# Performance work log

Measured on AMD Instinct MI355X. Metric: run time of the kernel, lower is better.

## Reference

```python
import jax, jax.numpy as jnp
import numpy as np

EPS = 1e-5


def gcn_conv(x, edge_index, W, b):
    # PyG GCNConv: h = x @ W; add self-loops; symmetric deg^-1/2 normalization; scatter-add to dst; + bias
    n = x.shape[0]
    h = x @ W  # [N, out]
    loops = jnp.arange(n, dtype=edge_index.dtype)
    src = jnp.concatenate([edge_index[0], loops])
    dst = jnp.concatenate([edge_index[1], loops])
    deg = jax.ops.segment_sum(jnp.ones(src.shape[0], dtype=h.dtype), dst, num_segments=n)
    dinv = jnp.where(deg > 0, jax.lax.rsqrt(jnp.maximum(deg, 1e-12)), 0.0)
    norm = dinv[src] * dinv[dst]  # [E+N]
    out = jax.ops.segment_sum(h[src] * norm[:, None], dst, num_segments=n)
    return out + b


def setup_inputs() -> dict:
    key = jax.random.key(0)
    ks = jax.random.split(key, 10)
    N, E = 50000, 800000
    IN, HID, OUT = 128, 128, 64
    x = jax.random.normal(ks[0], (N, IN), dtype=jnp.float32)
    edge_index1 = jax.random.randint(ks[1], (2, E), 0, N, dtype=jnp.int64)
    edge_index2 = jax.random.randint(ks[2], (2, E), 0, N, dtype=jnp.int64)
    s1 = 1.0 / np.sqrt(IN)
    s2 = 1.0 / np.sqrt(HID)
    W1 = jax.random.uniform(ks[3], (IN, HID), jnp.float32, -s1, s1)
    b1 = jax.random.uniform(ks[4], (HID,), jnp.float32, -s1, s1)
    gamma = jnp.ones((HID,), jnp.float32)
    beta = jnp.zeros((HID,), jnp.float32)
    W2 = jax.random.uniform(ks[5], (HID, OUT), jnp.float32, -s2, s2)
    b2 = jax.random.uniform(ks[6], (OUT,), jnp.float32, -s2, s2)
    return {"x": x, "edge_index1": edge_index1, "edge_index2": edge_index2,
            "W1": W1, "b1": b1, "gamma": gamma, "beta": beta, "W2": W2, "b2": b2}


def reference(x, edge_index1, edge_index2, W1, b1, gamma, beta, W2, b2):
    # layer 1: GCNConv -> (save hidden) -> BatchNorm1d (batch stats) -> ReLU -> dropout (identity, deterministic)
    h = gcn_conv(x, edge_index1, W1, b1)
    hidden = h
    mean = jnp.mean(h, axis=0)
    var = jnp.mean((h - mean) ** 2, axis=0)  # biased var, as torch BN uses for normalization
    h = (h - mean) * jax.lax.rsqrt(var + EPS) * gamma + beta
    h = jax.nn.relu(h)
    # layer 2: GCNConv (no norm/act on last layer)
    out = gcn_conv(h, edge_index2, W2, b2)
    return (out, hidden)
```

## Files before the change

kernel.cpp:

```cpp
#include <hip/hip_runtime.h>

#define GN 50000
#define GE 800000
#define HID 128
#define OUTC 64
#define NBK 196
#define NW  196
#define EPW 4096
#define PCAP 5888
#define A1B 2048

#define OFF_H1    0
#define OFF_H2    3200000
#define OFF_DINV1 4800000
#define OFF_DINV2 4850000
#define OFF_ROW1  4900000
#define OFF_ROW2  4950004
#define OFF_HIST  5000008
#define OFF_TOT   5076840
#define OFF_BBASE 5077232
#define OFF_BN    5077632
#define OFF_PART  5078144
#define OFF_PARTA 5602432
#define OFF_SRC1  5606528
#define OFF_SRC2  6406528

typedef __attribute__((ext_vector_type(8))) short bf16x8;
typedef __attribute__((ext_vector_type(4))) float f32x4;

__device__ inline unsigned bf16rne(float f) {
  unsigned u = __float_as_uint(f);
  return (u + 0x7FFFu + ((u >> 16) & 1u)) >> 16;
}
__device__ inline unsigned pack2(float a, float b) {
  return bf16rne(a) | (bf16rne(b) << 16);
}
__device__ inline float bflo(unsigned w) { return __uint_as_float(w << 16); }
__device__ inline float bfhi(unsigned w) { return __uint_as_float(w & 0xFFFF0000u); }
__device__ inline float bfs(unsigned short w) { return __uint_as_float(((unsigned)w) << 16); }

__global__ __launch_bounds__(256) void p1hist_kernel(const int* __restrict__ e1,
    const int* __restrict__ e2, int* __restrict__ hist) {
  __shared__ int h[NBK];
  int g = blockIdx.y, w = blockIdx.x;
  const int* dst = (g ? e2 : e1) + GE;
  for (int i = threadIdx.x; i < NBK; i += 256) h[i] = 0;
  __syncthreads();
  int i0 = w * EPW, iend = i0 + EPW; if (iend > GE) iend = GE;
  for (int i = i0 + threadIdx.x; i < iend; i += 256)
    atomicAdd(&h[dst[i] >> 8], 1);
  __syncthreads();
  int* out = hist + ((size_t)g * NW + w) * NBK;
  for (int i = threadIdx.x; i < NBK; i += 256) out[i] = h[i];
}

__global__ __launch_bounds__(256) void histscanA_kernel(int* __restrict__ hist,
    int* __restrict__ tot) {
  __shared__ int lds[256];
  int b = blockIdx.x, g = blockIdx.y, t = threadIdx.x;
  int* col = hist + (size_t)g * NW * NBK + b;
  int v = (t < NW) ? col[(size_t)t * NBK] : 0;
  lds[t] = v;
  __syncthreads();
  for (int off = 1; off < 256; off <<= 1) {
    int u = (t >= off) ? lds[t - off] : 0;
    __syncthreads();
    lds[t] += u;
    __syncthreads();
  }
  if (t < NW) col[(size_t)t * NBK] = lds[t] - v;
  if (t == NW - 1) tot[g * NBK + b] = lds[t];
}

__global__ __launch_bounds__(256) void histscanB_kernel(const int* __restrict__ tot,
    int* __restrict__ bbase) {
  __shared__ int lds[256];
  int t = threadIdx.x;
  for (int g = 0; g < 2; ++g) {
    int v = (t < NBK) ? tot[g * NBK + t] : 0;
    int orig = v;
    lds[t] = v;
    __syncthreads();
    for (int off = 1; off < 256; off <<= 1) {
      int u = (t >= off) ? lds[t - off] : 0;
      __syncthreads();
      lds[t] += u;
      __syncthreads();
    }
    if (t < NBK) bbase[g * (NBK + 1) + t] = lds[t] - orig;
    if (t == NBK - 1) bbase[g * (NBK + 1) + NBK] = lds[t];
    __syncthreads();
  }
}

__global__ __launch_bounds__(256) void p1scat_kernel(const int* __restrict__ e1,
    const int* __restrict__ e2, const int* __restrict__ hist,
    const int* __restrict__ bbase, int* __restrict__ pb1, int* __restrict__ pb2) {
  __shared__ int off[NBK];
  int g = blockIdx.y, w = blockIdx.x;
  const int* e = g ? e2 : e1;
  int* pb = g ? pb2 : pb1;
  const int* hrow = hist + ((size_t)g * NW + w) * NBK;
  const int* bb = bbase + g * (NBK + 1);
  for (int i = threadIdx.x; i < NBK; i += 256) off[i] = bb[i] + hrow[i];
  __syncthreads();
  int i0 = w * EPW, iend = i0 + EPW; if (iend > GE) iend = GE;
  for (int i = i0 + threadIdx.x; i < iend; i += 256) {
    int d = e[GE + i], s = e[i];
    int p = atomicAdd(&off[d >> 8], 1);
    pb[p] = s | ((d & 255) << 16);
  }
}

__global__ __launch_bounds__(256) void p2sort_kernel(const int* __restrict__ pb1,
    const int* __restrict__ pb2, const int* __restrict__ bbase,
    int* __restrict__ row1, int* __restrict__ row2,
    float* __restrict__ dinv1, float* __restrict__ dinv2,
    int* __restrict__ src1, int* __restrict__ src2) {
  __shared__ int stage[PCAP];
  __shared__ int lcnt[256], lc2[256], arr[256];
  __shared__ int lrow[257];
  int g = blockIdx.y, b = blockIdx.x, t = threadIdx.x;
  const int* pb = g ? pb2 : pb1;
  const int* bb = bbase + g * (NBK + 1);
  int* row = g ? row2 : row1;
  float* dinv = g ? dinv2 : dinv1;
  int* src = g ? src2 : src1;
  int lo = b << 8, hi = lo + 256; if (hi > GN) hi = GN;
  int nn = hi - lo;
  int base = bb[b], end = bb[b + 1], L = end - base;
  lcnt[t] = 0; lc2[t] = 0;
  __syncthreads();
  for (int i = base + t; i < end; i += 256)
    atomicAdd(&lcnt[((unsigned)pb[i]) >> 16], 1);
  __syncthreads();
  int v = lcnt[t];
  arr[t] = v;
  __syncthreads();
  for (int off = 1; off < 256; off <<= 1) {
    int u = (t >= off) ? arr[t - off] : 0;
    __syncthreads();
    arr[t] += u;
    __syncthreads();
  }
  lrow[t] = arr[t] - v;
  if (t == 255) lrow[256] = arr[255];
  __syncthreads();
  if (t < nn) {
    row[lo + t] = base + lrow[t];
    dinv[lo + t] = rsqrtf(1.0f + (float)lcnt[t]);
  }
  if (b == NBK - 1 && t == 0) row[GN] = end;
  if (L <= PCAP) {
    for (int i = base + t; i < end; i += 256) {
      unsigned p = (unsigned)pb[i];
      int ld = p >> 16;
      int rk = atomicAdd(&lc2[ld], 1);
      stage[lrow[ld] + rk] = (int)(p & 0xFFFFu);
    }
    __syncthreads();
    for (int i = t; i < L; i += 256) src[base + i] = stage[i];
  } else {
    for (int i = base + t; i < end; i += 256) {
      unsigned p = (unsigned)pb[i];
      int ld = p >> 16;
      int rk = atomicAdd(&lc2[ld], 1);
      src[base + lrow[ld] + rk] = (int)(p & 0xFFFFu);
    }
  }
}

__global__ __launch_bounds__(256) void gemm1_kernel(const float* __restrict__ A,
    const float* __restrict__ W1, const float* __restrict__ dinv1,
    unsigned short* __restrict__ h1u) {
  __shared__ unsigned a_lds[64 * 68];
  __shared__ unsigned w_lds[128 * 68];
  int t = threadIdx.x;
  int row0 = blockIdx.x * 64;
  for (int i = t; i < 128 * 64; i += 256) {
    int k2 = i >> 7, n = i & 127;
    w_lds[n * 68 + k2] = pack2(W1[(2 * k2) * 128 + n], W1[(2 * k2 + 1) * 128 + n]);
  }
  for (int i = t; i < 64 * 32; i += 256) {
    int m = i >> 5, k4 = i & 31;
    int gr = row0 + m;
    float4 v = (gr < GN) ? ((const float4*)A)[(size_t)gr * 32 + k4]
                         : make_float4(0.f, 0.f, 0.f, 0.f);
    unsigned* dst = &a_lds[m * 68 + k4 * 2];
    dst[0] = pack2(v.x, v.y);
    dst[1] = pack2(v.z, v.w);
  }
  __syncthreads();
  int lane = t & 63, w = t >> 6;
  int n16 = lane & 15, quad = lane >> 4;
  int mbase = (w & 1) * 32;
  int nbase = (w >> 1) * 64;
  f32x4 acc[2][4] = {};
  const unsigned short* als = (const unsigned short*)a_lds;
  const unsigned short* wls = (const unsigned short*)w_lds;
  #pragma unroll
  for (int ks = 0; ks < 4; ++ks) {
    int k0 = ks * 32 + quad * 8;
    bf16x8 a0 = *(const bf16x8*)(als + (mbase + n16) * 136 + k0);
    bf16x8 a1 = *(const bf16x8*)(als + (mbase + 16 + n16) * 136 + k0);
    #pragma unroll
    for (int nt = 0; nt < 4; ++nt) {
      bf16x8 bf = *(const bf16x8*)(wls + (nbase + nt * 16 + n16) * 136 + k0);
      acc[0][nt] = __builtin_amdgcn_mfma_f32_16x16x32_bf16(a0, bf, acc[0][nt], 0, 0, 0);
      acc[1][nt] = __builtin_amdgcn_mfma_f32_16x16x32_bf16(a1, bf, acc[1][nt], 0, 0, 0);
    }
  }
  #pragma unroll
  for (int mt = 0; mt < 2; ++mt) {
    #pragma unroll
    for (int r = 0; r < 4; ++r) {
      int row_g = row0 + mbase + mt * 16 + quad * 4 + r;
      if (row_g < GN) {
        float dv = dinv1[row_g];
        #pragma unroll
        for (int nt = 0; nt < 4; ++nt) {
          int col = nbase + nt * 16 + n16;
          h1u[(size_t)row_g * 128 + col] = (unsigned short)bf16rne(dv * acc[mt][nt][r]);
        }
      }
    }
  }
}

__global__ __launch_bounds__(256) void gemm2_kernel(const float* __restrict__ A,
    const float* __restrict__ W2, const float* __restrict__ scale,
    const float* __restrict__ shift, const float* __restrict__ dinv2,
    unsigned short* __restrict__ h2u) {
  __shared__ unsigned a_lds[64 * 68];
  __shared__ unsigned w_lds[64 * 68];
  __shared__ float sc[128], sh[128];
  int t = threadIdx.x;
  if (t < 128) { sc[t] = scale[t]; sh[t] = shift[t]; }
  int row0 = blockIdx.x * 64;
  for (int i = t; i < 64 * 64; i += 256) {
    int k2 = i >> 6, n = i & 63;
    w_lds[n * 68 + k2] = pack2(W2[(2 * k2) * 64 + n], W2[(2 * k2 + 1) * 64 + n]);
  }
  __syncthreads();
  for (int i = t; i < 64 * 32; i += 256) {
    int m = i >> 5, k4 = i & 31;
    int gr = row0 + m;
    float4 v = (gr < GN) ? ((const float4*)A)[(size_t)gr * 32 + k4]
                         : make_float4(0.f, 0.f, 0.f, 0.f);
    int c = k4 * 4;
    v.x = fmaxf(fmaf(v.x, sc[c],     sh[c]),     0.f);
    v.y = fmaxf(fmaf(v.y, sc[c + 1], sh[c + 1]), 0.f);
    v.z = fmaxf(fmaf(v.z, sc[c + 2], sh[c + 2]), 0.f);
    v.w = fmaxf(fmaf(v.w, sc[c + 3], sh[c + 3]), 0.f);
    unsigned* dst = &a_lds[m * 68 + k4 * 2];
    dst[0] = pack2(v.x, v.y);
    dst[1] = pack2(v.z, v.w);
  }
  __syncthreads();
  int lane = t & 63, w = t >> 6;
  int n16 = lane & 15, quad = lane >> 4;
  f32x4 acc[4] = {};
  const unsigned short* als = (const unsigned short*)a_lds;
  const unsigned short* wls = (const unsigned short*)w_lds;
  #pragma unroll
  for (int ks = 0; ks < 4; ++ks) {
    int k0 = ks * 32 + quad * 8;
    bf16x8 af = *(const bf16x8*)(als + (w * 16 + n16) * 136 + k0);
    #pragma unroll
    for (int nt = 0; nt < 4; ++nt) {
      bf16x8 bf = *(const bf16x8*)(wls + (nt * 16 + n16) * 136 + k0);
      acc[nt] = __builtin_amdgcn_mfma_f32_16x16x32_bf16(af, bf, acc[nt], 0, 0, 0);
    }
  }
  #pragma unroll
  for (int r = 0; r < 4; ++r) {
    int row_g = row0 + w * 16 + quad * 4 + r;
    if (row_g < GN) {
      float dv = dinv2[row_g];
      #pragma unroll
      for (int nt = 0; nt < 4; ++nt) {
        int col = nt * 16 + n16;
        h2u[(size_t)row_g * 64 + col] = (unsigned short)bf16rne(dv * acc[nt][r]);
      }
    }
  }
}

__global__ __launch_bounds__(256) void agg1_kernel(const unsigned* __restrict__ h1b,
    const int* __restrict__ row, const int* __restrict__ srcs,
    const float* __restrict__ dinv, const float* __restrict__ b1,
    float* __restrict__ hidden, float* __restrict__ part) {
  __shared__ float ps[256];
  int t = threadIdx.x;
  int lane = t & 63;
  float2 b = ((const float2*)b1)[lane];
  float sx = 0.f, sy = 0.f, qx = 0.f, qy = 0.f;
  int wid = (blockIdx.x * 256 + t) >> 6;
  for (int d = wid; d < GN; d += A1B * 4) {
    float di = dinv[d];
    unsigned sw = h1b[(size_t)d * 64 + lane];
    float ax = bflo(sw), ay = bfhi(sw);
    int e0 = row[d], e1 = row[d + 1];
    int i = e0;
    while ((i & 3) && i < e1) {
      unsigned v = h1b[(size_t)srcs[i] * 64 + lane];
      ax += bflo(v); ay += bfhi(v);
      ++i;
    }
    for (; i + 8 <= e1; i += 8) {
      int4 sa = *(const int4*)&srcs[i];
      int4 sb = *(const int4*)&srcs[i + 4];
      unsigned v0 = h1b[(size_t)sa.x * 64 + lane], v1 = h1b[(size_t)sa.y * 64 + lane];
      unsigned v2 = h1b[(size_t)sa.z * 64 + lane], v3 = h1b[(size_t)sa.w * 64 + lane];
      unsigned v4 = h1b[(size_t)sb.x * 64 + lane], v5 = h1b[(size_t)sb.y * 64 + lane];
      unsigned v6 = h1b[(size_t)sb.z * 64 + lane], v7 = h1b[(size_t)sb.w * 64 + lane];
      ax += bflo(v0); ay += bfhi(v0);
      ax += bflo(v1); ay += bfhi(v1);
      ax += bflo(v2); ay += bfhi(v2);
      ax += bflo(v3); ay += bfhi(v3);
      ax += bflo(v4); ay += bfhi(v4);
      ax += bflo(v5); ay += bfhi(v5);
      ax += bflo(v6); ay += bfhi(v6);
      ax += bflo(v7); ay += bfhi(v7);
    }
    if (i + 4 <= e1) {
      int4 sa = *(const int4*)&srcs[i];
      unsigned v0 = h1b[(size_t)sa.x * 64 + lane], v1 = h1b[(size_t)sa.y * 64 + lane];
      unsigned v2 = h1b[(size_t)sa.z * 64 + lane], v3 = h1b[(size_t)sa.w * 64 + lane];
      ax += bflo(v0); ay += bfhi(v0);
      ax += bflo(v1); ay += bfhi(v1);
      ax += bflo(v2); ay += bfhi(v2);
      ax += bflo(v3); ay += bfhi(v3);
      i += 4;
    }
    for (; i < e1; ++i) {
      unsigned v = h1b[(size_t)srcs[i] * 64 + lane];
      ax += bflo(v); ay += bfhi(v);
    }
    float ox = ax * di + b.x, oy = ay * di + b.y;
    float2 o; o.x = ox; o.y = oy;
    ((float2*)(hidden + (size_t)d * 128))[lane] = o;
    sx += ox; sy += oy; qx += ox * ox; qy += oy * oy;
  }
  float* pout = part + (size_t)blockIdx.x * 256;
  ps[t] = sx; __syncthreads();
  if (t < 64) pout[2 * t] = ps[t] + ps[t + 64] + ps[t + 128] + ps[t + 192];
  __syncthreads();
  ps[t] = sy; __syncthreads();
  if (t < 64) pout[2 * t + 1] = ps[t] + ps[t + 64] + ps[t + 128] + ps[t + 192];
  __syncthreads();
  ps[t] = qx; __syncthreads();
  if (t < 64) pout[128 + 2 * t] = ps[t] + ps[t + 64] + ps[t + 128] + ps[t + 192];
  __syncthreads();
  ps[t] = qy; __syncthreads();
  if (t < 64) pout[128 + 2 * t + 1] = ps[t] + ps[t + 64] + ps[t + 128] + ps[t + 192];
}

__global__ __launch_bounds__(256) void bn_reduceA_kernel(const float* __restrict__ part,
    float* __restrict__ partA) {
  int r = blockIdx.x, t = threadIdx.x;
  float s = 0.f;
  for (int k = 0; k < A1B / 16; ++k)
    s += part[((size_t)r * (A1B / 16) + k) * 256 + t];
  partA[r * 256 + t] = s;
}

__global__ __launch_bounds__(128) void bn_final_kernel(const float* __restrict__ partA,
    const float* __restrict__ gamma, const float* __restrict__ beta,
    float* __restrict__ scale, float* __restrict__ shift) {
  int c = threadIdx.x;
  float S = 0.f, Q = 0.f;
  for (int r = 0; r < 16; ++r) {
    S += partA[r * 256 + c];
    Q += partA[r * 256 + 128 + c];
  }
  float mean = S * (1.0f / GN);
  float var = Q * (1.0f / GN) - mean * mean;
  float istd = rsqrtf(var + 1e-5f);
  float g = gamma[c] * istd;
  scale[c] = g;
  shift[c] = beta[c] - mean * g;
}

__global__ __launch_bounds__(256) void agg2_kernel(const unsigned short* __restrict__ h2b,
    const int* __restrict__ row, const int* __restrict__ srcs,
    const float* __restrict__ dinv, const float* __restrict__ b2,
    float* __restrict__ out) {
  int wave = (blockIdx.x * 256 + threadIdx.x) >> 6;
  int lane = threadIdx.x & 63;
  if (wave >= GN) return;
  int d = wave;
  float di = dinv[d];
  float acc = bfs(h2b[(size_t)d * 64 + lane]);
  int e0 = row[d], e1 = row[d + 1];
  int i = e0;
  while ((i & 3) && i < e1) {
    acc += bfs(h2b[(size_t)srcs[i] * 64 + lane]);
    ++i;
  }
  for (; i + 8 <= e1; i += 8) {
    int4 sa = *(const int4*)&srcs[i];
    int4 sb = *(const int4*)&srcs[i + 4];
    float v0 = bfs(h2b[(size_t)sa.x * 64 + lane]), v1 = bfs(h2b[(size_t)sa.y * 64 + lane]);
    float v2 = bfs(h2b[(size_t)sa.z * 64 + lane]), v3 = bfs(h2b[(size_t)sa.w * 64 + lane]);
    float v4 = bfs(h2b[(size_t)sb.x * 64 + lane]), v5 = bfs(h2b[(size_t)sb.y * 64 + lane]);
    float v6 = bfs(h2b[(size_t)sb.z * 64 + lane]), v7 = bfs(h2b[(size_t)sb.w * 64 + lane]);
    acc += v0 + v1 + v2 + v3 + v4 + v5 + v6 + v7;
  }
  if (i + 4 <= e1) {
    int4 sa = *(const int4*)&srcs[i];
    acc += bfs(h2b[(size_t)sa.x * 64 + lane]) + bfs(h2b[(size_t)sa.y * 64 + lane])
         + bfs(h2b[(size_t)sa.z * 64 + lane]) + bfs(h2b[(size_t)sa.w * 64 + lane]);
    i += 4;
  }
  for (; i < e1; ++i)
    acc += bfs(h2b[(size_t)srcs[i] * 64 + lane]);
  out[(size_t)d * 64 + lane] = acc * di + b2[lane];
}

extern "C" void kernel_launch(void* const* d_in, const int* in_sizes, int n_in,
                              void* d_out, int out_size, void* d_ws, size_t ws_size,
                              hipStream_t stream) {
  const float* x     = (const float*)d_in[0];
  const int*   e1    = (const int*)d_in[1];
  const int*   e2    = (const int*)d_in[2];
  const float* W1    = (const float*)d_in[3];
  const float* b1    = (const float*)d_in[4];
  const float* gamma = (const float*)d_in[5];
  const float* beta  = (const float*)d_in[6];
  const float* W2    = (const float*)d_in[7];
  const float* b2    = (const float*)d_in[8];

  float* out    = (float*)d_out;
  float* hidden = out + (size_t)GN * OUTC;

  float*          ws    = (float*)d_ws;
  unsigned*       h1b   = (unsigned*)(ws + OFF_H1);
  unsigned*       h2b   = (unsigned*)(ws + OFF_H2);
  float*          dinv1 = ws + OFF_DINV1;
  float*          dinv2 = ws + OFF_DINV2;
  int*            row1  = (int*)(ws + OFF_ROW1);
  int*            row2  = (int*)(ws + OFF_ROW2);
  int*            hist  = (int*)(ws + OFF_HIST);
  int*            tot   = (int*)(ws + OFF_TOT);
  int*            bbase = (int*)(ws + OFF_BBASE);
  float*          bnbuf = ws + OFF_BN;
  float*          part  = ws + OFF_PART;
  float*          partA = ws + OFF_PARTA;
  int*            src1  = (int*)(ws + OFF_SRC1);
  int*            src2  = (int*)(ws + OFF_SRC2);
  int*            pb1   = (int*)h2b;
  int*            pb2   = pb1 + GE;

  p1hist_kernel<<<dim3(NW, 2), 256, 0, stream>>>(e1, e2, hist);
  histscanA_kernel<<<dim3(NBK, 2), 256, 0, stream>>>(hist, tot);
  histscanB_kernel<<<1, 256, 0, stream>>>(tot, bbase);
  p1scat_kernel<<<dim3(NW, 2), 256, 0, stream>>>(e1, e2, hist, bbase, pb1, pb2);
  p2sort_kernel<<<dim3(NBK, 2), 256, 0, stream>>>(pb1, pb2, bbase,
                                                  row1, row2, dinv1, dinv2, src1, src2);

  gemm1_kernel<<<(GN + 63) / 64, 256, 0, stream>>>(x, W1, dinv1,
                                                   (unsigned short*)h1b);
  agg1_kernel<<<A1B, 256, 0, stream>>>(h1b, row1, src1, dinv1, b1, hidden, part);

  bn_reduceA_kernel<<<16, 256, 0, stream>>>(part, partA);
  bn_final_kernel<<<1, 128, 0, stream>>>(partA, gamma, beta, bnbuf, bnbuf + 128);

  gemm2_kernel<<<(GN + 63) / 64, 256, 0, stream>>>(hidden, W2, bnbuf, bnbuf + 128,
                                                   dinv2, (unsigned short*)h2b);
  agg2_kernel<<<(GN * 64 + 255) / 256, 256, 0, stream>>>(
      (const unsigned short*)h2b, row2, src2, dinv2, b2, out);
}
```

Measured before the change: 229.5 us.

## Fold scan and BN-finalize kernels into neighbors; unroll agg1 gather by 16

Removes the single-block histscanB kernel by having the last-finishing histscanA block (tracked by an atomic counter reset in p1hist) compute the bucket bases. The bn_final kernel is dropped and each gemm2 block recomputes scale and shift from partA. The agg1 neighbor gather loop is widened to 16 loads in flight per iteration. These cut two launches and their serialization gaps and raise memory-level parallelism, at the cost of redundant BN math per gemm2 block and threadfence/atomic overhead.

```diff
diff --git a/kernel.cpp b/kernel.cpp
--- a/kernel.cpp
+++ b/kernel.cpp
@@ -40,9 +40,10 @@
 __device__ inline float bfs(unsigned short w) { return __uint_as_float(((unsigned)w) << 16); }
 
 __global__ __launch_bounds__(256) void p1hist_kernel(const int* __restrict__ e1,
-    const int* __restrict__ e2, int* __restrict__ hist) {
+    const int* __restrict__ e2, int* __restrict__ hist, int* __restrict__ scnt) {
   __shared__ int h[NBK];
   int g = blockIdx.y, w = blockIdx.x;
+  if (g == 0 && w == 0 && threadIdx.x == 0) *scnt = 0;
   const int* dst = (g ? e2 : e1) + GE;
   for (int i = threadIdx.x; i < NBK; i += 256) h[i] = 0;
   __syncthreads();
@@ -55,8 +56,9 @@
 }
 
 __global__ __launch_bounds__(256) void histscanA_kernel(int* __restrict__ hist,
-    int* __restrict__ tot) {
+    int* __restrict__ tot, int* __restrict__ bbase, int* __restrict__ scnt) {
   __shared__ int lds[256];
+  __shared__ bool last;
   int b = blockIdx.x, g = blockIdx.y, t = threadIdx.x;
   int* col = hist + (size_t)g * NW * NBK + b;
   int v = (t < NW) ? col[(size_t)t * NBK] : 0;
@@ -70,16 +72,16 @@
   }
   if (t < NW) col[(size_t)t * NBK] = lds[t] - v;
   if (t == NW - 1) tot[g * NBK + b] = lds[t];
-}
-
-__global__ __launch_bounds__(256) void histscanB_kernel(const int* __restrict__ tot,
-    int* __restrict__ bbase) {
-  __shared__ int lds[256];
-  int t = threadIdx.x;
-  for (int g = 0; g < 2; ++g) {
-    int v = (t < NBK) ? tot[g * NBK + t] : 0;
-    int orig = v;
-    lds[t] = v;
+  __threadfence();
+  __syncthreads();
+  if (t == 0) last = (atomicAdd(scnt, 1) == 2 * NBK - 1);
+  __syncthreads();
+  if (!last) return;
+  __threadfence();
+  for (int gg = 0; gg < 2; ++gg) {
+    int v2 = (t < NBK) ? tot[gg * NBK + t] : 0;
+    int orig = v2;
+    lds[t] = v2;
     __syncthreads();
     for (int off = 1; off < 256; off <<= 1) {
       int u = (t >= off) ? lds[t - off] : 0;
@@ -87,8 +89,8 @@
       lds[t] += u;
       __syncthreads();
     }
-    if (t < NBK) bbase[g * (NBK + 1) + t] = lds[t] - orig;
-    if (t == NBK - 1) bbase[g * (NBK + 1) + NBK] = lds[t];
+    if (t < NBK) bbase[gg * (NBK + 1) + t] = lds[t] - orig;
+    if (t == NBK - 1) bbase[gg * (NBK + 1) + NBK] = lds[t];
     __syncthreads();
   }
 }
@@ -228,14 +230,27 @@
 }
 
 __global__ __launch_bounds__(256) void gemm2_kernel(const float* __restrict__ A,
-    const float* __restrict__ W2, const float* __restrict__ scale,
-    const float* __restrict__ shift, const float* __restrict__ dinv2,
-    unsigned short* __restrict__ h2u) {
+    const float* __restrict__ W2, const float* __restrict__ partA,
+    const float* __restrict__ gamma, const float* __restrict__ beta,
+    const float* __restrict__ dinv2, unsigned short* __restrict__ h2u) {
   __shared__ unsigned a_lds[64 * 68];
   __shared__ unsigned w_lds[64 * 68];
   __shared__ float sc[128], sh[128];
   int t = threadIdx.x;
-  if (t < 128) { sc[t] = scale[t]; sh[t] = shift[t]; }
+  if (t < 128) {
+    float S = 0.f, Q = 0.f;
+    #pragma unroll
+    for (int r = 0; r < 16; ++r) {
+      S += partA[r * 256 + t];
+      Q += partA[r * 256 + 128 + t];
+    }
+    float mean = S * (1.0f / GN);
+    float var = Q * (1.0f / GN) - mean * mean;
+    float istd = rsqrtf(var + 1e-5f);
+    float g = gamma[t] * istd;
+    sc[t] = g;
+    sh[t] = beta[t] - mean * g;
+  }
   int row0 = blockIdx.x * 64;
   for (int i = t; i < 64 * 64; i += 256) {
     int k2 = i >> 6, n = i & 63;
@@ -307,7 +322,37 @@
       ax += bflo(v); ay += bfhi(v);
       ++i;
     }
-    for (; i + 8 <= e1; i += 8) {
+    for (; i + 16 <= e1; i += 16) {
+      int4 sa = *(const int4*)&srcs[i];
+      int4 sb = *(const int4*)&srcs[i + 4];
+      int4 sc4 = *(const int4*)&srcs[i + 8];
+      int4 sd = *(const int4*)&srcs[i + 12];
+      unsigned v0 = h1b[(size_t)sa.x * 64 + lane],  v1 = h1b[(size_t)sa.y * 64 + lane];
+      unsigned v2 = h1b[(size_t)sa.z * 64 + lane],  v3 = h1b[(size_t)sa.w * 64 + lane];
+      unsigned v4 = h1b[(size_t)sb.x * 64 + lane],  v5 = h1b[(size_t)sb.y * 64 + lane];
+      unsigned v6 = h1b[(size_t)sb.z * 64 + lane],  v7 = h1b[(size_t)sb.w * 64 + lane];
+      unsigned v8 = h1b[(size_t)sc4.x * 64 + lane], v9 = h1b[(size_t)sc4.y * 64 + lane];
+      unsigned va = h1b[(size_t)sc4.z * 64 + lane], vb = h1b[(size_t)sc4.w * 64 + lane];
+      unsigned vc = h1b[(size_t)sd.x * 64 + lane],  vd = h1b[(size_t)sd.y * 64 + lane];
+      unsigned ve = h1b[(size_t)sd.z * 64 + lane],  vf = h1b[(size_t)sd.w * 64 + lane];
+      ax += bflo(v0); ay += bfhi(v0);
+      ax += bflo(v1); ay += bfhi(v1);
+      ax += bflo(v2); ay += bfhi(v2);
+      ax += bflo(v3); ay += bfhi(v3);
+      ax += bflo(v4); ay += bfhi(v4);
+      ax += bflo(v5); ay += bfhi(v5);
+      ax += bflo(v6); ay += bfhi(v6);
+      ax += bflo(v7); ay += bfhi(v7);
+      ax += bflo(v8); ay += bfhi(v8);
+      ax += bflo(v9); ay += bfhi(v9);
+      ax += bflo(va); ay += bfhi(va);
+      ax += bflo(vb); ay += bfhi(vb);
+      ax += bflo(vc); ay += bfhi(vc);
+      ax += bflo(vd); ay += bfhi(vd);
+      ax += bflo(ve); ay += bfhi(ve);
+      ax += bflo(vf); ay += bfhi(vf);
+    }
+    if (i + 8 <= e1) {
       int4 sa = *(const int4*)&srcs[i];
       int4 sb = *(const int4*)&srcs[i + 4];
       unsigned v0 = h1b[(size_t)sa.x * 64 + lane], v1 = h1b[(size_t)sa.y * 64 + lane];
@@ -322,6 +367,7 @@
       ax += bflo(v5); ay += bfhi(v5);
       ax += bflo(v6); ay += bfhi(v6);
       ax += bflo(v7); ay += bfhi(v7);
+      i += 8;
     }
     if (i + 4 <= e1) {
       int4 sa = *(const int4*)&srcs[i];
@@ -363,23 +409,6 @@
   for (int k = 0; k < A1B / 16; ++k)
     s += part[((size_t)r * (A1B / 16) + k) * 256 + t];
   partA[r * 256 + t] = s;
-}
-
-__global__ __launch_bounds__(128) void bn_final_kernel(const float* __restrict__ partA,
-    const float* __restrict__ gamma, const float* __restrict__ beta,
-    float* __restrict__ scale, float* __restrict__ shift) {
-  int c = threadIdx.x;
-  float S = 0.f, Q = 0.f;
-  for (int r = 0; r < 16; ++r) {
-    S += partA[r * 256 + c];
-    Q += partA[r * 256 + 128 + c];
-  }
-  float mean = S * (1.0f / GN);
-  float var = Q * (1.0f / GN) - mean * mean;
-  float istd = rsqrtf(var + 1e-5f);
-  float g = gamma[c] * istd;
-  scale[c] = g;
-  shift[c] = beta[c] - mean * g;
 }
 
 __global__ __launch_bounds__(256) void agg2_kernel(const unsigned short* __restrict__ h2b,
@@ -445,6 +474,7 @@
   int*            tot   = (int*)(ws + OFF_TOT);
   int*            bbase = (int*)(ws + OFF_BBASE);
   float*          bnbuf = ws + OFF_BN;
+  int*            scnt  = (int*)(bnbuf + 384);
   float*          part  = ws + OFF_PART;
   float*          partA = ws + OFF_PARTA;
   int*            src1  = (int*)(ws + OFF_SRC1);
@@ -452,9 +482,8 @@
   int*            pb1   = (int*)h2b;
   int*            pb2   = pb1 + GE;
 
-  p1hist_kernel<<<dim3(NW, 2), 256, 0, stream>>>(e1, e2, hist);
-  histscanA_kernel<<<dim3(NBK, 2), 256, 0, stream>>>(hist, tot);
-  histscanB_kernel<<<1, 256, 0, stream>>>(tot, bbase);
+  p1hist_kernel<<<dim3(NW, 2), 256, 0, stream>>>(e1, e2, hist, scnt);
+  histscanA_kernel<<<dim3(NBK, 2), 256, 0, stream>>>(hist, tot, bbase, scnt);
   p1scat_kernel<<<dim3(NW, 2), 256, 0, stream>>>(e1, e2, hist, bbase, pb1, pb2);
   p2sort_kernel<<<dim3(NBK, 2), 256, 0, stream>>>(pb1, pb2, bbase,
                                                   row1, row2, dinv1, dinv2, src1, src2);
@@ -464,9 +493,8 @@
   agg1_kernel<<<A1B, 256, 0, stream>>>(h1b, row1, src1, dinv1, b1, hidden, part);
 
   bn_reduceA_kernel<<<16, 256, 0, stream>>>(part, partA);
-  bn_final_kernel<<<1, 128, 0, stream>>>(partA, gamma, beta, bnbuf, bnbuf + 128);
-
-  gemm2_kernel<<<(GN + 63) / 64, 256, 0, stream>>>(hidden, W2, bnbuf, bnbuf + 128,
+
+  gemm2_kernel<<<(GN + 63) / 64, 256, 0, stream>>>(hidden, W2, partA, gamma, beta,
                                                    dinv2, (unsigned short*)h2b);
   agg2_kernel<<<(GN * 64 + 255) / 256, 256, 0, stream>>>(
       (const unsigned short*)h2b, row2, src2, dinv2, b2, out);
```

New measurement: 281.5 us. 1.23x slower.
